# Kernel tuning notes

Measured on AMD Instinct MI355X. Metric: run time of the kernel, lower is better.

## Reference

```python
import jax, jax.numpy as jnp
import numpy as np

B, T, C = 4, 2048, 1024
NH = 16
HD = C // NH  # 64


def setup_inputs() -> dict:
    key = jax.random.key(0)
    k1, k2, k3, k4, k5 = jax.random.split(key, 5)
    s_in = 1.0 / np.sqrt(C)
    return {
        "x": jax.random.normal(k1, (B, T, C), dtype=jnp.float32),
        "attention_mask": jnp.ones((B, T), dtype=jnp.float32),
        "W_qkv": jax.random.normal(k2, (C, 3 * C), dtype=jnp.float32) * s_in,
        "b_qkv": jnp.zeros((3 * C,), dtype=jnp.float32),
        "W_out": jax.random.normal(k3, (C, C), dtype=jnp.float32) * s_in,
        "b_out": jnp.zeros((C,), dtype=jnp.float32),
    }


def reference(x, attention_mask, W_qkv, b_qkv, W_out, b_out):
    Bx, Tx, Cx = x.shape
    # QKV projection: (B,T,3C)
    qkv = x @ W_qkv + b_qkv
    Q, K, V = jnp.split(qkv, 3, axis=-1)
    # (B, NH, T, HD)
    Q = Q.reshape(Bx, Tx, NH, HD).transpose(0, 2, 1, 3)
    K = K.reshape(Bx, Tx, NH, HD).transpose(0, 2, 1, 3)
    V = V.reshape(Bx, Tx, NH, HD).transpose(0, 2, 1, 3)
    # scaled scores (B, NH, T, T)
    scores = jnp.einsum("bhqd,bhkd->bhqk", Q, K) * (1.0 / np.sqrt(HD))
    # causal mask: set strictly-upper triangle to -inf (mask-fill semantics)
    causal = jnp.tril(jnp.ones((Tx, Tx), dtype=bool))[None, None]
    scores = jnp.where(causal, scores, -jnp.inf)
    # additive padding mask
    pad = (1.0 - attention_mask)[:, None, None, :] * jnp.finfo(scores.dtype).min
    scores = scores + pad
    attn = jax.nn.softmax(scores, axis=-1)
    # weighted values -> (B, T, C)
    wv = jnp.einsum("bhqk,bhkd->bhqd", attn, V)
    wv = wv.transpose(0, 2, 1, 3).reshape(Bx, Tx, Cx)
    return wv @ W_out + b_out
```

## Files before the change

kernel.cpp:

```cpp
#include <hip/hip_runtime.h>
#include <math.h>

constexpr int BB = 4;
constexpr int TT = 2048;
constexpr int CC = 1024;
constexpr int NHH = 16;
constexpr int HDD = 64;
constexpr int C3 = 3 * CC;

typedef __bf16 bf16x8 __attribute__((ext_vector_type(8)));
typedef __bf16 bf16x4 __attribute__((ext_vector_type(4)));
typedef float  f32x4  __attribute__((ext_vector_type(4)));

__device__ __forceinline__ unsigned short f2bf(float x) {
    union { float f; unsigned u; } v; v.f = x;
    unsigned r = v.u + 0x7fffu + ((v.u >> 16) & 1u);
    return (unsigned short)(r >> 16);
}

#define AS1(p) ((const __attribute__((address_space(1))) void*)(p))
#define AS3(p) ((__attribute__((address_space(3))) void*)(p))

constexpr float SM2 = 17.312340490667561f;

constexpr int CAST_BLOCKS = (BB * TT * CC / 4) / 256;
constexpr int TQKV_BLOCKS = (C3 / 64) * (CC / 64);
constexpr int TOUT_BLOCKS = (CC / 64) * (CC / 64);
constexpr int KB_BLOCKS   = (BB * TT) / 256;

__global__ __launch_bounds__(256) void prep(
    const float* __restrict__ x,
    const float* __restrict__ Wqkv,
    const float* __restrict__ Wout,
    const float* __restrict__ amask,
    unsigned short* __restrict__ xb,
    unsigned short* __restrict__ Wqkvt,
    unsigned short* __restrict__ Woutt,
    float* __restrict__ kbias)
{
    __shared__ float tile[64][65];
    const int bid = blockIdx.x;
    const int t = threadIdx.x;

    if (bid < CAST_BLOCKS) {
        const int i = bid * 256 + t;
        float4 v = ((const float4*)x)[i];
        ushort4 o;
        o.x = f2bf(v.x); o.y = f2bf(v.y); o.z = f2bf(v.z); o.w = f2bf(v.w);
        ((ushort4*)xb)[i] = o;
        return;
    }
    if (bid >= CAST_BLOCKS + TQKV_BLOCKS + TOUT_BLOCKS) {
        const int i = (bid - CAST_BLOCKS - TQKV_BLOCKS - TOUT_BLOCKS) * 256 + t;
        kbias[i] = (amask[i] - 1.0f) * 1.0e38f - SM2;
        return;
    }

    const float* src; unsigned short* dst; int R, Cn, r0, c0;
    if (bid < CAST_BLOCKS + TQKV_BLOCKS) {
        const int tb = bid - CAST_BLOCKS;
        src = Wqkv; dst = Wqkvt; R = CC; Cn = C3;
        c0 = (tb % (C3 / 64)) * 64; r0 = (tb / (C3 / 64)) * 64;
    } else {
        const int tb = bid - CAST_BLOCKS - TQKV_BLOCKS;
        src = Wout; dst = Woutt; R = CC; Cn = CC;
        c0 = (tb % (CC / 64)) * 64; r0 = (tb / (CC / 64)) * 64;
    }

    const int lr = t >> 4, lc = (t & 15) * 4;
    #pragma unroll
    for (int s = 0; s < 4; ++s) {
        float4 v = *(const float4*)&src[(size_t)(r0 + lr + s * 16) * Cn + c0 + lc];
        tile[lr + s * 16][lc + 0] = v.x;
        tile[lr + s * 16][lc + 1] = v.y;
        tile[lr + s * 16][lc + 2] = v.z;
        tile[lr + s * 16][lc + 3] = v.w;
    }
    __syncthreads();
    const int oi = t >> 2, oc = (t & 3) * 16;
    unsigned short buf[16];
    #pragma unroll
    for (int u = 0; u < 16; ++u)
        buf[u] = f2bf(tile[oc + u][oi]);
    unsigned short* d = &dst[(size_t)(c0 + oi) * R + r0 + oc];
    *(uint4*)(d + 0) = *(uint4*)&buf[0];
    *(uint4*)(d + 8) = *(uint4*)&buf[8];
}

template<bool VSPLIT>
__global__ __launch_bounds__(256, 2) void gemm_bt_mfma(
    const unsigned short* __restrict__ A,
    const unsigned short* __restrict__ Bt,
    const float* __restrict__ bias,
    float* __restrict__ OutF,
    unsigned short* __restrict__ Qp,
    unsigned short* __restrict__ Kp,
    unsigned short* __restrict__ Vtp,
    int M, int N, int K, float qscale)
{
    __shared__ alignas(16) unsigned short As[2][128 * 64];
    __shared__ alignas(16) unsigned short Bs[2][128 * 64];

    const int tid  = threadIdx.x;
    const int w    = tid >> 6;
    const int lane = tid & 63;
    const int quad = lane >> 4;
    const int col  = lane & 15;

    const int nX  = gridDim.x;
    const int lin = blockIdx.y * nX + blockIdx.x;
    const int pos = lin >> 3;
    const int mt  = ((lin & 7) << 3) | (pos & 7);
    const int nt  = pos >> 3;
    const int m0 = mt * 128, n0 = nt * 128;
    const int wr = w >> 1, wc = w & 1;

    f32x4 acc[4][4];
    #pragma unroll
    for (int i = 0; i < 4; ++i)
        #pragma unroll
        for (int j = 0; j < 4; ++j)
            #pragma unroll
            for (int r = 0; r < 4; ++r)
                acc[i][j][r] = 0.0f;

    const int srow = tid >> 3;
    const int spos = tid & 7;
    char* AsB = (char*)&As[0][0];
    char* BsB = (char*)&Bs[0][0];

    const int nk = K >> 6;

    auto DMA = [&](int kt, int buf) {
        const int k0 = kt << 6;
        #pragma unroll
        for (int i = 0; i < 4; ++i) {
            const int row = srow + 32 * i;
            const int sch = spos ^ (row & 7);
            __builtin_amdgcn_global_load_lds(
                AS1(A + (size_t)(m0 + row) * K + k0 + sch * 8),
                AS3(AsB + buf * 16384 + i * 4096 + w * 1024), 16, 0, 0);
            __builtin_amdgcn_global_load_lds(
                AS1(Bt + (size_t)(n0 + row) * K + k0 + sch * 8),
                AS3(BsB + buf * 16384 + i * 4096 + w * 1024), 16, 0, 0);
        }
    };

    DMA(0, 0);
    DMA(1, 1);
    asm volatile("s_waitcnt vmcnt(8)" ::: "memory");
    __builtin_amdgcn_s_barrier();

    for (int kt = 0; kt < nk; ++kt) {
        const int cur = kt & 1;
        const unsigned short* as = &As[cur][0];
        const unsigned short* bs = &Bs[cur][0];

        #pragma unroll
        for (int ks = 0; ks < 2; ++ks) {
            bf16x8 af[4], bf[4];
            #pragma unroll
            for (int i = 0; i < 4; ++i) {
                const int ra = wr * 64 + i * 16 + col;
                const int pa = ((quad + ks * 4) ^ (ra & 7)) * 8;
                af[i] = *(const bf16x8*)&as[ra * 64 + pa];
                const int rb = wc * 64 + i * 16 + col;
                const int pb = ((quad + ks * 4) ^ (rb & 7)) * 8;
                bf[i] = *(const bf16x8*)&bs[rb * 64 + pb];
            }
            #pragma unroll
            for (int i = 0; i < 4; ++i)
                #pragma unroll
                for (int j = 0; j < 4; ++j)
                    acc[i][j] = __builtin_amdgcn_mfma_f32_16x16x32_bf16(af[i], bf[j], acc[i][j], 0, 0, 0);
        }

        __builtin_amdgcn_s_barrier();
        if (kt + 2 < nk) {
            DMA(kt + 2, cur);
            asm volatile("s_waitcnt vmcnt(8)" ::: "memory");
        } else {
            asm volatile("s_waitcnt vmcnt(0)" ::: "memory");
        }
        __builtin_amdgcn_s_barrier();
    }

    if (VSPLIT) {
        if (n0 < CC) {
            #pragma unroll
            for (int i = 0; i < 4; ++i)
                #pragma unroll
                for (int r = 0; r < 4; ++r) {
                    const int m = m0 + wr * 64 + i * 16 + quad * 4 + r;
                    #pragma unroll
                    for (int j = 0; j < 4; ++j) {
                        const int n = n0 + wc * 64 + j * 16 + col;
                        Qp[(size_t)m * CC + n] = f2bf((acc[i][j][r] + bias[n]) * qscale);
                    }
                }
        } else if (n0 < 2 * CC) {
            #pragma unroll
            for (int i = 0; i < 4; ++i) {
                const int mb   = m0 + wr * 64 + i * 16 + quad * 4;
                const int bidx = mb >> 11;
                const int tloc = mb & 2047;
                #pragma unroll
                for (int j = 0; j < 4; ++j) {
                    const int n  = n0 + wc * 64 + j * 16 + col;
                    const int hh = (n - CC) >> 6;
                    const int dd = (n - CC) & 63;
                    #pragma unroll
                    for (int r = 0; r < 4; ++r)
                        Kp[(((size_t)bidx * NHH + hh) * TT + tloc + r) * HDD + dd] =
                            f2bf(acc[i][j][r] + bias[n]);
                }
            }
        } else {
            #pragma unroll
            for (int i = 0; i < 4; ++i) {
                const int mb   = m0 + wr * 64 + i * 16 + quad * 4;
                const int bidx = mb >> 11;
                const int tloc = mb & 2047;
                const int ktile = tloc >> 6, tc = tloc & 63;
                #pragma unroll
                for (int j = 0; j < 4; ++j) {
                    const int n  = n0 + wc * 64 + j * 16 + col;
                    const int hh = (n - 2 * CC) >> 6;
                    const int dd = (n - 2 * CC) & 63;
                    unsigned short pk[4];
                    #pragma unroll
                    for (int r = 0; r < 4; ++r)
                        pk[r] = f2bf(acc[i][j][r] + bias[n]);
                    *(uint2*)&Vtp[((((size_t)bidx * NHH + hh) * 32 + ktile) * HDD + dd) * 64 + tc] =
                        *(const uint2*)pk;
                }
            }
        }
    } else {
        #pragma unroll
        for (int i = 0; i < 4; ++i)
            #pragma unroll
            for (int r = 0; r < 4; ++r) {
                const int m = m0 + wr * 64 + i * 16 + quad * 4 + r;
                #pragma unroll
                for (int j = 0; j < 4; ++j) {
                    const int n = n0 + wc * 64 + j * 16 + col;
                    OutF[(size_t)m * N + n] = acc[i][j][r] + bias[n];
                }
            }
    }
}

constexpr int PP = 72;

__global__ __launch_bounds__(256, 3) void attn_mfma(
    const unsigned short* __restrict__ Qp,
    const unsigned short* __restrict__ Kp,
    const unsigned short* __restrict__ Vtp,
    const float* __restrict__ kbias,
    unsigned short* __restrict__ WV)
{
    __shared__ alignas(16) unsigned short Ks [2][64 * 64];
    __shared__ alignas(16) unsigned short Vts[2][64 * 64];
    __shared__ alignas(16) __bf16        Ps[4][32 * PP];

    const int tid  = threadIdx.x;
    const int w    = tid >> 6;
    const int lane = tid & 63;
    const int quad = lane >> 4;
    const int col  = lane & 15;

    const int gi = blockIdx.x;
    const int j  = gi >> 3;
    const int bh = ((gi & 7) << 3) | (j & 7);
    const int qb = 15 - (j >> 3);
    const int b = bh >> 4, h = bh & 15;

    const unsigned short* Qg = Qp + (size_t)b * TT * CC + (size_t)h * HDD;
    const unsigned short* Kg = Kp + (size_t)bh * TT * HDD;
    const unsigned short* Vg = Vtp + (size_t)bh * 32 * HDD * 64;
    const float* kb_g = kbias + b * TT;

    const int srow = tid >> 3;
    const int sch  = (tid & 7) ^ (srow & 7);
    char* KsB  = (char*)&Ks[0][0];
    char* VtsB = (char*)&Vts[0][0];

    const int qw = qb * 128 + w * 32;
    const int ntiles = 2 * qb + 2;

    bf16x8 qfa0 = *(const bf16x8*)(Qg + (size_t)(qw + col) * CC + quad * 8);
    bf16x8 qfa1 = *(const bf16x8*)(Qg + (size_t)(qw + col) * CC + 32 + quad * 8);
    bf16x8 qfb0 = *(const bf16x8*)(Qg + (size_t)(qw + 16 + col) * CC + quad * 8);
    bf16x8 qfb1 = *(const bf16x8*)(Qg + (size_t)(qw + 16 + col) * CC + 32 + quad * 8);

    f32x4 o[2][4];
    float l[2] = {0.0f, 0.0f};
    #pragma unroll
    for (int hh = 0; hh < 2; ++hh)
        #pragma unroll
        for (int t = 0; t < 4; ++t)
            #pragma unroll
            for (int r = 0; r < 4; ++r) o[hh][t][r] = 0.0f;

    auto DMA = [&](int tile, int buf) {
        #pragma unroll
        for (int i = 0; i < 2; ++i) {
            __builtin_amdgcn_global_load_lds(
                AS1(Kg + (size_t)(tile * 64 + srow + 32 * i) * HDD + sch * 8),
                AS3(KsB + buf * 8192 + i * 4096 + w * 1024), 16, 0, 0);
            __builtin_amdgcn_global_load_lds(
                AS1(Vg + ((size_t)tile * 64 + srow + 32 * i) * 64 + sch * 8),
                AS3(VtsB + buf * 8192 + i * 4096 + w * 1024), 16, 0, 0);
        }
    };

    f32x4 kbc[4], kbn[4];
    DMA(0, 0);
    #pragma unroll
    for (int t = 0; t < 4; ++t)
        kbc[t] = *(const f32x4*)&kb_g[t * 16 + quad * 4];
    DMA(1, 1);
    #pragma unroll
    for (int t = 0; t < 4; ++t)
        kbn[t] = *(const f32x4*)&kb_g[64 + t * 16 + quad * 4];
    asm volatile("s_waitcnt vmcnt(8)" ::: "memory");
    __builtin_amdgcn_s_barrier();

    for (int it = 0; it < ntiles; ++it) {
        const int kt  = it << 6;
        const int cur = it & 1;

        if (kt <= qw + 31) {
            const unsigned short* ksb = &Ks[cur][0];
            const unsigned short* vsb = &Vts[cur][0];

            f32x4 s[2][4];
            #pragma unroll
            for (int t = 0; t < 4; ++t) {
                const int row = t * 16 + col;
                const int c0 = (quad ^ (row & 7)) * 8;
                const int c1 = ((quad + 4) ^ (row & 7)) * 8;
                bf16x8 k0 = *(const bf16x8*)&ksb[row * 64 + c0];
                bf16x8 k1 = *(const bf16x8*)&ksb[row * 64 + c1];
                f32x4 za = __builtin_amdgcn_mfma_f32_16x16x32_bf16(k0, qfa0, kbc[t], 0, 0, 0);
                za = __builtin_amdgcn_mfma_f32_16x16x32_bf16(k1, qfa1, za, 0, 0, 0);
                s[0][t] = za;
                f32x4 zb = __builtin_amdgcn_mfma_f32_16x16x32_bf16(k0, qfb0, kbc[t], 0, 0, 0);
                zb = __builtin_amdgcn_mfma_f32_16x16x32_bf16(k1, qfb1, zb, 0, 0, 0);
                s[1][t] = zb;
            }

            const bool needc = (kt + 64 > qw);
            #pragma unroll
            for (int hh = 0; hh < 2; ++hh) {
                const int q = qw + hh * 16 + col;
                #pragma unroll
                for (int t = 0; t < 4; ++t) {
                    float pv[4];
                    #pragma unroll
                    for (int r = 0; r < 4; ++r) {
                        const int key = kt + t * 16 + quad * 4 + r;
                        float p = __builtin_amdgcn_exp2f(s[hh][t][r]);
                        if (needc && key > q) p = 0.0f;
                        l[hh] += p;
                        pv[r] = p;
                    }
                    bf16x4 pk4 = { (__bf16)pv[0], (__bf16)pv[1],
                                   (__bf16)pv[2], (__bf16)pv[3] };
                    *(bf16x4*)&Ps[w][(hh * 16 + col) * PP + t * 16 + quad * 4] = pk4;
                }
            }

            bf16x8 pa0 = *(const bf16x8*)&Ps[w][col * PP + quad * 8];
            bf16x8 pa1 = *(const bf16x8*)&Ps[w][col * PP + 32 + quad * 8];
            bf16x8 pb0 = *(const bf16x8*)&Ps[w][(16 + col) * PP + quad * 8];
            bf16x8 pb1 = *(const bf16x8*)&Ps[w][(16 + col) * PP + 32 + quad * 8];
            #pragma unroll
            for (int t = 0; t < 4; ++t) {
                const int row = t * 16 + col;
                const int c0 = (quad ^ (row & 7)) * 8;
                const int c1 = ((quad + 4) ^ (row & 7)) * 8;
                bf16x8 v0 = *(const bf16x8*)&vsb[row * 64 + c0];
                bf16x8 v1 = *(const bf16x8*)&vsb[row * 64 + c1];
                o[0][t] = __builtin_amdgcn_mfma_f32_16x16x32_bf16(pa0, v0, o[0][t], 0, 0, 0);
                o[0][t] = __builtin_amdgcn_mfma_f32_16x16x32_bf16(pa1, v1, o[0][t], 0, 0, 0);
                o[1][t] = __builtin_amdgcn_mfma_f32_16x16x32_bf16(pb0, v0, o[1][t], 0, 0, 0);
                o[1][t] = __builtin_amdgcn_mfma_f32_16x16x32_bf16(pb1, v1, o[1][t], 0, 0, 0);
            }
        }

        __builtin_amdgcn_s_barrier();

        #pragma unroll
        for (int t = 0; t < 4; ++t) kbc[t] = kbn[t];

        if (it + 2 < ntiles) {
            DMA(it + 2, cur);
            #pragma unroll
            for (int t = 0; t < 4; ++t)
                kbn[t] = *(const f32x4*)&kb_g[(it + 2) * 64 + t * 16 + quad * 4];
            asm volatile("s_waitcnt vmcnt(8)" ::: "memory");
        } else {
            asm volatile("s_waitcnt vmcnt(0)" ::: "memory");
        }
        __builtin_amdgcn_s_barrier();
    }

    #pragma unroll
    for (int hh = 0; hh < 2; ++hh) {
        l[hh] += __shfl_xor(l[hh], 16);
        l[hh] += __shfl_xor(l[hh], 32);
    }
    #pragma unroll
    for (int hh = 0; hh < 2; ++hh) {
        #pragma unroll
        for (int r = 0; r < 4; ++r) {
            const float Lr = __shfl(l[hh], (lane & 48) | (quad * 4 + r));
            const float inv = 1.0f / Lr;
            const int q = qw + hh * 16 + quad * 4 + r;
            unsigned short* dst = WV + ((size_t)b * TT + q) * CC + (size_t)h * HDD;
            #pragma unroll
            for (int t = 0; t < 4; ++t)
                dst[t * 16 + col] = f2bf(o[hh][t][r] * inv);
        }
    }
}

extern "C" void kernel_launch(void* const* d_in, const int* in_sizes, int n_in,
                              void* d_out, int out_size, void* d_ws, size_t ws_size,
                              hipStream_t stream) {
    const float* x     = (const float*)d_in[0];
    const float* amask = (const float*)d_in[1];
    const float* Wqkv  = (const float*)d_in[2];
    const float* bqkv  = (const float*)d_in[3];
    const float* Wout  = (const float*)d_in[4];
    const float* bout  = (const float*)d_in[5];
    float* out = (float*)d_out;

    const int M = BB * TT;

    unsigned short* xb    = (unsigned short*)d_ws;
    unsigned short* Wqkvt = xb    + (size_t)M * CC;
    unsigned short* Woutt = Wqkvt + (size_t)C3 * CC;
    unsigned short* Qp    = Woutt + (size_t)CC * CC;
    unsigned short* Kp    = Qp    + (size_t)M * CC;
    unsigned short* Vtp   = Kp    + (size_t)M * CC;
    unsigned short* wvb   = Vtp   + (size_t)M * CC;
    float*          kbias = (float*)(wvb + (size_t)M * CC);

    dim3 blk(256);

    prep<<<dim3(CAST_BLOCKS + TQKV_BLOCKS + TOUT_BLOCKS + KB_BLOCKS), blk, 0, stream>>>(
        x, Wqkv, Wout, amask, xb, Wqkvt, Woutt, kbias);

    gemm_bt_mfma<true><<<dim3(C3 / 128, M / 128), blk, 0, stream>>>(
        xb, Wqkvt, bqkv, nullptr, Qp, Kp, Vtp, M, C3, CC, 0.18033688011112043f);
    attn_mfma<<<dim3(1024), dim3(256), 0, stream>>>(
        Qp, Kp, Vtp, kbias, wvb);
    gemm_bt_mfma<false><<<dim3(CC / 128, M / 128), blk, 0, stream>>>(
        wvb, Woutt, bout, out, nullptr, nullptr, nullptr, M, CC, CC, 1.0f);
}
```

Measured before the change: 234.7 us.

## Load GEMM B operand directly from global into registers, bypassing LDS

The GEMM kernel no longer stages the B tile through shared memory. Each wave loads its own 64-column slice of B straight into register fragments one k-tile ahead, using ping-pong register buffers and a loop unrolled by two. This halves LDS traffic and footprint, and the LDS reads of B go away. In exchange it costs more VGPRs and issues less coalesced global loads, since both waves in a row pair fetch their B slices separately. The vmcnt waits are also retuned, and their counting with the mixed load types is fragile.

```diff
diff --git a/kernel.cpp b/kernel.cpp
--- a/kernel.cpp
+++ b/kernel.cpp
@@ -99,7 +99,6 @@
     int M, int N, int K, float qscale)
 {
     __shared__ alignas(16) unsigned short As[2][128 * 64];
-    __shared__ alignas(16) unsigned short Bs[2][128 * 64];
 
     const int tid  = threadIdx.x;
     const int w    = tid >> 6;
@@ -127,63 +126,89 @@
     const int srow = tid >> 3;
     const int spos = tid & 7;
     char* AsB = (char*)&As[0][0];
-    char* BsB = (char*)&Bs[0][0];
 
     const int nk = K >> 6;
+
+    const unsigned short* Bw = Bt + (size_t)(n0 + wc * 64) * K;
 
     auto DMA = [&](int kt, int buf) {
         const int k0 = kt << 6;
         #pragma unroll
         for (int i = 0; i < 4; ++i) {
             const int row = srow + 32 * i;
-            const int sch = spos ^ (row & 7);
+            const int sc = spos ^ (row & 7);
             __builtin_amdgcn_global_load_lds(
-                AS1(A + (size_t)(m0 + row) * K + k0 + sch * 8),
+                AS1(A + (size_t)(m0 + row) * K + k0 + sc * 8),
                 AS3(AsB + buf * 16384 + i * 4096 + w * 1024), 16, 0, 0);
-            __builtin_amdgcn_global_load_lds(
-                AS1(Bt + (size_t)(n0 + row) * K + k0 + sch * 8),
-                AS3(BsB + buf * 16384 + i * 4096 + w * 1024), 16, 0, 0);
         }
     };
 
+    #define LOADB(dst, T) { \
+        const int kk0 = ((T) << 6); \
+        _Pragma("unroll") \
+        for (int j = 0; j < 4; ++j) { \
+            const unsigned short* bp = Bw + (size_t)(j * 16 + col) * K + kk0 + quad * 8; \
+            dst[j * 2 + 0] = *(const bf16x8*)(bp); \
+            dst[j * 2 + 1] = *(const bf16x8*)(bp + 32); \
+        } }
+
+    #define COMPUTE(buf, bfr) { \
+        const unsigned short* as = &As[buf][0]; \
+        _Pragma("unroll") \
+        for (int ks = 0; ks < 2; ++ks) { \
+            bf16x8 af[4]; \
+            _Pragma("unroll") \
+            for (int i = 0; i < 4; ++i) { \
+                const int ra = wr * 64 + i * 16 + col; \
+                const int pa = ((quad + ks * 4) ^ (ra & 7)) * 8; \
+                af[i] = *(const bf16x8*)&as[ra * 64 + pa]; \
+            } \
+            _Pragma("unroll") \
+            for (int i = 0; i < 4; ++i) \
+                _Pragma("unroll") \
+                for (int j = 0; j < 4; ++j) \
+                    acc[i][j] = __builtin_amdgcn_mfma_f32_16x16x32_bf16(af[i], bfr[j * 2 + ks], acc[i][j], 0, 0, 0); \
+        } }
+
+    bf16x8 bfA[8], bfB[8];
+
+    LOADB(bfA, 0);
     DMA(0, 0);
     DMA(1, 1);
-    asm volatile("s_waitcnt vmcnt(8)" ::: "memory");
+    asm volatile("s_waitcnt vmcnt(4)" ::: "memory");
     __builtin_amdgcn_s_barrier();
 
-    for (int kt = 0; kt < nk; ++kt) {
-        const int cur = kt & 1;
-        const unsigned short* as = &As[cur][0];
-        const unsigned short* bs = &Bs[cur][0];
-
-        #pragma unroll
-        for (int ks = 0; ks < 2; ++ks) {
-            bf16x8 af[4], bf[4];
-            #pragma unroll
-            for (int i = 0; i < 4; ++i) {
-                const int ra = wr * 64 + i * 16 + col;
-                const int pa = ((quad + ks * 4) ^ (ra & 7)) * 8;
-                af[i] = *(const bf16x8*)&as[ra * 64 + pa];
-                const int rb = wc * 64 + i * 16 + col;
-                const int pb = ((quad + ks * 4) ^ (rb & 7)) * 8;
-                bf[i] = *(const bf16x8*)&bs[rb * 64 + pb];
-            }
-            #pragma unroll
-            for (int i = 0; i < 4; ++i)
-                #pragma unroll
-                for (int j = 0; j < 4; ++j)
-                    acc[i][j] = __builtin_amdgcn_mfma_f32_16x16x32_bf16(af[i], bf[j], acc[i][j], 0, 0, 0);
-        }
-
+    for (int kt = 0; kt < nk; kt += 2) {
+        if (kt + 1 < nk) LOADB(bfB, kt + 1);
+        COMPUTE(0, bfA);
         __builtin_amdgcn_s_barrier();
         if (kt + 2 < nk) {
-            DMA(kt + 2, cur);
+            DMA(kt + 2, 0);
+            asm volatile("s_waitcnt vmcnt(12)" ::: "memory");
+        } else if (kt + 1 < nk) {
             asm volatile("s_waitcnt vmcnt(8)" ::: "memory");
         } else {
             asm volatile("s_waitcnt vmcnt(0)" ::: "memory");
         }
         __builtin_amdgcn_s_barrier();
-    }
+
+        if (kt + 1 < nk) {
+            if (kt + 2 < nk) LOADB(bfA, kt + 2);
+            COMPUTE(1, bfB);
+            __builtin_amdgcn_s_barrier();
+            if (kt + 3 < nk) {
+                DMA(kt + 3, 1);
+                asm volatile("s_waitcnt vmcnt(12)" ::: "memory");
+            } else if (kt + 2 < nk) {
+                asm volatile("s_waitcnt vmcnt(8)" ::: "memory");
+            } else {
+                asm volatile("s_waitcnt vmcnt(0)" ::: "memory");
+            }
+            __builtin_amdgcn_s_barrier();
+        }
+    }
+    #undef LOADB
+    #undef COMPUTE
 
     if (VSPLIT) {
         if (n0 < CC) {
```

Result: slower. 308.6 us (+31.5%).

## Use 128x256 tiles with per-wave full-M layout in QKV GEMM

Applied to the files above, without the earlier changes.

The QKV projection GEMM gets its own kernel with a 128x256 output tile, where each wave owns a 128x64 column strip (8x4 MFMA accumulators) instead of a 64x64 quadrant. The wider tile halves the block count to 768 and raises arithmetic intensity per LDS byte, and the block-to-tile mapping groups M tiles by XCD for L2 reuse. The cost is 48KB LDS per buffer pair, launch bounds of 1 block per CU, and roughly 128 accumulator registers per thread, which lowers occupancy and latency hiding. The output GEMM is split off as a separate non-templated kernel with unchanged behaviour.

```diff
diff --git a/kernel.cpp b/kernel.cpp
--- a/kernel.cpp
+++ b/kernel.cpp
@@ -22,6 +22,7 @@
 #define AS3(p) ((__attribute__((address_space(3))) void*)(p))
 
 constexpr float SM2 = 17.312340490667561f;
+constexpr float QSCALE = 0.18033688011112043f;
 
 constexpr int CAST_BLOCKS = (BB * TT * CC / 4) / 256;
 constexpr int TQKV_BLOCKS = (C3 / 64) * (CC / 64);
@@ -87,16 +88,164 @@
     *(uint4*)(d + 8) = *(uint4*)&buf[8];
 }
 
-template<bool VSPLIT>
-__global__ __launch_bounds__(256, 2) void gemm_bt_mfma(
+__global__ __launch_bounds__(256, 1) void gemm_qkv(
+    const unsigned short* __restrict__ A,
+    const unsigned short* __restrict__ Bt,
+    const float* __restrict__ bias,
+    unsigned short* __restrict__ Qp,
+    unsigned short* __restrict__ Kp,
+    unsigned short* __restrict__ Vtp)
+{
+    __shared__ alignas(16) unsigned short As[2][128 * 64];
+    __shared__ alignas(16) unsigned short Bs[2][256 * 64];
+
+    const int tid  = threadIdx.x;
+    const int w    = tid >> 6;
+    const int lane = tid & 63;
+    const int quad = lane >> 4;
+    const int col  = lane & 15;
+
+    const int lin = blockIdx.x;
+    const int xcd = lin & 7, idx = lin >> 3;
+    const int mt  = xcd * 8 + (idx & 7);
+    const int nt  = idx >> 3;
+    const int m0 = mt * 128, n0 = nt * 256;
+
+    f32x4 acc[8][4];
+    #pragma unroll
+    for (int i = 0; i < 8; ++i)
+        #pragma unroll
+        for (int j = 0; j < 4; ++j)
+            #pragma unroll
+            for (int r = 0; r < 4; ++r)
+                acc[i][j][r] = 0.0f;
+
+    const int srow8 = lane >> 3;
+    const int sch   = (lane & 7) ^ srow8;
+    char* AsB = (char*)&As[0][0];
+    char* BsB = (char*)&Bs[0][0];
+
+    constexpr int K  = CC;
+    constexpr int nk = K / 64;
+
+    auto STAGE = [&](int kt, int buf) {
+        const int k0 = kt << 6;
+        #pragma unroll
+        for (int i = 0; i < 4; ++i) {
+            const int row = w * 32 + i * 8 + srow8;
+            __builtin_amdgcn_global_load_lds(
+                AS1(A + (size_t)(m0 + row) * K + k0 + sch * 8),
+                AS3(AsB + buf * 16384 + w * 4096 + i * 1024), 16, 0, 0);
+        }
+        #pragma unroll
+        for (int i = 0; i < 8; ++i) {
+            const int row = w * 64 + i * 8 + srow8;
+            __builtin_amdgcn_global_load_lds(
+                AS1(Bt + (size_t)(n0 + row) * K + k0 + sch * 8),
+                AS3(BsB + buf * 32768 + w * 8192 + i * 1024), 16, 0, 0);
+        }
+    };
+
+    STAGE(0, 0);
+    STAGE(1, 1);
+    asm volatile("s_waitcnt vmcnt(12)" ::: "memory");
+    __builtin_amdgcn_s_barrier();
+
+    for (int kt = 0; kt < nk; ++kt) {
+        const int cur = kt & 1;
+        const unsigned short* as = &As[cur][0];
+        const unsigned short* bs = &Bs[cur][0];
+
+        #pragma unroll
+        for (int ks = 0; ks < 2; ++ks) {
+            bf16x8 af[8], bf[4];
+            #pragma unroll
+            for (int i = 0; i < 8; ++i) {
+                const int ra = i * 16 + col;
+                const int pa = ((quad + ks * 4) ^ (ra & 7)) * 8;
+                af[i] = *(const bf16x8*)&as[ra * 64 + pa];
+            }
+            #pragma unroll
+            for (int j = 0; j < 4; ++j) {
+                const int rb = w * 64 + j * 16 + col;
+                const int pb = ((quad + ks * 4) ^ (rb & 7)) * 8;
+                bf[j] = *(const bf16x8*)&bs[rb * 64 + pb];
+            }
+            #pragma unroll
+            for (int i = 0; i < 8; ++i)
+                #pragma unroll
+                for (int j = 0; j < 4; ++j)
+                    acc[i][j] = __builtin_amdgcn_mfma_f32_16x16x32_bf16(af[i], bf[j], acc[i][j], 0, 0, 0);
+        }
+
+        __builtin_amdgcn_s_barrier();
+        if (kt + 2 < nk) {
+            STAGE(kt + 2, cur);
+            asm volatile("s_waitcnt vmcnt(12)" ::: "memory");
+        } else {
+            asm volatile("s_waitcnt vmcnt(0)" ::: "memory");
+        }
+        __builtin_amdgcn_s_barrier();
+    }
+
+    if (n0 < CC) {
+        #pragma unroll
+        for (int i = 0; i < 8; ++i)
+            #pragma unroll
+            for (int r = 0; r < 4; ++r) {
+                const int m = m0 + i * 16 + quad * 4 + r;
+                #pragma unroll
+                for (int j = 0; j < 4; ++j) {
+                    const int n = n0 + w * 64 + j * 16 + col;
+                    Qp[(size_t)m * CC + n] = f2bf((acc[i][j][r] + bias[n]) * QSCALE);
+                }
+            }
+    } else if (n0 < 2 * CC) {
+        #pragma unroll
+        for (int i = 0; i < 8; ++i) {
+            const int mb   = m0 + i * 16 + quad * 4;
+            const int bidx = mb >> 11;
+            const int tloc = mb & 2047;
+            #pragma unroll
+            for (int j = 0; j < 4; ++j) {
+                const int n  = n0 + w * 64 + j * 16 + col;
+                const int hh = (n - CC) >> 6;
+                const int dd = (n - CC) & 63;
+                #pragma unroll
+                for (int r = 0; r < 4; ++r)
+                    Kp[(((size_t)bidx * NHH + hh) * TT + tloc + r) * HDD + dd] =
+                        f2bf(acc[i][j][r] + bias[n]);
+            }
+        }
+    } else {
+        #pragma unroll
+        for (int i = 0; i < 8; ++i) {
+            const int mb   = m0 + i * 16 + quad * 4;
+            const int bidx = mb >> 11;
+            const int tloc = mb & 2047;
+            const int ktile = tloc >> 6, tc = tloc & 63;
+            #pragma unroll
+            for (int j = 0; j < 4; ++j) {
+                const int n  = n0 + w * 64 + j * 16 + col;
+                const int hh = (n - 2 * CC) >> 6;
+                const int dd = (n - 2 * CC) & 63;
+                unsigned short pk[4];
+                #pragma unroll
+                for (int r = 0; r < 4; ++r)
+                    pk[r] = f2bf(acc[i][j][r] + bias[n]);
+                *(uint2*)&Vtp[((((size_t)bidx * NHH + hh) * 32 + ktile) * HDD + dd) * 64 + tc] =
+                    *(const uint2*)pk;
+            }
+        }
+    }
+}
+
+__global__ __launch_bounds__(256, 2) void gemm_out(
     const unsigned short* __restrict__ A,
     const unsigned short* __restrict__ Bt,
     const float* __restrict__ bias,
     float* __restrict__ OutF,
-    unsigned short* __restrict__ Qp,
-    unsigned short* __restrict__ Kp,
-    unsigned short* __restrict__ Vtp,
-    int M, int N, int K, float qscale)
+    int M, int N, int K)
 {
     __shared__ alignas(16) unsigned short As[2][128 * 64];
     __shared__ alignas(16) unsigned short Bs[2][128 * 64];
@@ -136,12 +285,12 @@
         #pragma unroll
         for (int i = 0; i < 4; ++i) {
             const int row = srow + 32 * i;
-            const int sch = spos ^ (row & 7);
+            const int sc = spos ^ (row & 7);
             __builtin_amdgcn_global_load_lds(
-                AS1(A + (size_t)(m0 + row) * K + k0 + sch * 8),
+                AS1(A + (size_t)(m0 + row) * K + k0 + sc * 8),
                 AS3(AsB + buf * 16384 + i * 4096 + w * 1024), 16, 0, 0);
             __builtin_amdgcn_global_load_lds(
-                AS1(Bt + (size_t)(n0 + row) * K + k0 + sch * 8),
+                AS1(Bt + (size_t)(n0 + row) * K + k0 + sc * 8),
                 AS3(BsB + buf * 16384 + i * 4096 + w * 1024), 16, 0, 0);
         }
     };
@@ -185,70 +334,17 @@
         __builtin_amdgcn_s_barrier();
     }
 
-    if (VSPLIT) {
-        if (n0 < CC) {
-            #pragma unroll
-            for (int i = 0; i < 4; ++i)
-                #pragma unroll
-                for (int r = 0; r < 4; ++r) {
-                    const int m = m0 + wr * 64 + i * 16 + quad * 4 + r;
-                    #pragma unroll
-                    for (int j = 0; j < 4; ++j) {
-                        const int n = n0 + wc * 64 + j * 16 + col;
-                        Qp[(size_t)m * CC + n] = f2bf((acc[i][j][r] + bias[n]) * qscale);
-                    }
-                }
-        } else if (n0 < 2 * CC) {
-            #pragma unroll
-            for (int i = 0; i < 4; ++i) {
-                const int mb   = m0 + wr * 64 + i * 16 + quad * 4;
-                const int bidx = mb >> 11;
-                const int tloc = mb & 2047;
-                #pragma unroll
-                for (int j = 0; j < 4; ++j) {
-                    const int n  = n0 + wc * 64 + j * 16 + col;
-                    const int hh = (n - CC) >> 6;
-                    const int dd = (n - CC) & 63;
-                    #pragma unroll
-                    for (int r = 0; r < 4; ++r)
-                        Kp[(((size_t)bidx * NHH + hh) * TT + tloc + r) * HDD + dd] =
-                            f2bf(acc[i][j][r] + bias[n]);
-                }
-            }
-        } else {
-            #pragma unroll
-            for (int i = 0; i < 4; ++i) {
-                const int mb   = m0 + wr * 64 + i * 16 + quad * 4;
-                const int bidx = mb >> 11;
-                const int tloc = mb & 2047;
-                const int ktile = tloc >> 6, tc = tloc & 63;
-                #pragma unroll
-                for (int j = 0; j < 4; ++j) {
-                    const int n  = n0 + wc * 64 + j * 16 + col;
-                    const int hh = (n - 2 * CC) >> 6;
-                    const int dd = (n - 2 * CC) & 63;
-                    unsigned short pk[4];
-                    #pragma unroll
-                    for (int r = 0; r < 4; ++r)
-                        pk[r] = f2bf(acc[i][j][r] + bias[n]);
-                    *(uint2*)&Vtp[((((size_t)bidx * NHH + hh) * 32 + ktile) * HDD + dd) * 64 + tc] =
-                        *(const uint2*)pk;
-                }
-            }
-        }
-    } else {
-        #pragma unroll
-        for (int i = 0; i < 4; ++i)
-            #pragma unroll
-            for (int r = 0; r < 4; ++r) {
-                const int m = m0 + wr * 64 + i * 16 + quad * 4 + r;
-                #pragma unroll
-                for (int j = 0; j < 4; ++j) {
-                    const int n = n0 + wc * 64 + j * 16 + col;
-                    OutF[(size_t)m * N + n] = acc[i][j][r] + bias[n];
-                }
-            }
-    }
+    #pragma unroll
+    for (int i = 0; i < 4; ++i)
+        #pragma unroll
+        for (int r = 0; r < 4; ++r) {
+            const int m = m0 + wr * 64 + i * 16 + quad * 4 + r;
+            #pragma unroll
+            for (int j = 0; j < 4; ++j) {
+                const int n = n0 + wc * 64 + j * 16 + col;
+                OutF[(size_t)m * N + n] = acc[i][j][r] + bias[n];
+            }
+        }
 }
 
 constexpr int PP = 72;
@@ -454,10 +550,10 @@
     prep<<<dim3(CAST_BLOCKS + TQKV_BLOCKS + TOUT_BLOCKS + KB_BLOCKS), blk, 0, stream>>>(
         x, Wqkv, Wout, amask, xb, Wqkvt, Woutt, kbias);
 
-    gemm_bt_mfma<true><<<dim3(C3 / 128, M / 128), blk, 0, stream>>>(
-        xb, Wqkvt, bqkv, nullptr, Qp, Kp, Vtp, M, C3, CC, 0.18033688011112043f);
+    gemm_qkv<<<dim3(768), blk, 0, stream>>>(
+        xb, Wqkvt, bqkv, Qp, Kp, Vtp);
     attn_mfma<<<dim3(1024), dim3(256), 0, stream>>>(
         Qp, Kp, Vtp, kbias, wvb);
-    gemm_bt_mfma<false><<<dim3(CC / 128, M / 128), blk, 0, stream>>>(
-        wvb, Woutt, bout, out, nullptr, nullptr, nullptr, M, CC, CC, 1.0f);
+    gemm_out<<<dim3(CC / 128, M / 128), blk, 0, stream>>>(
+        wvb, Woutt, bout, out, M, CC, CC);
 }
```

Measured after the change: 270.4 us. 1.15x slower.

## Double attention block to 8 waves over 256 queries sharing K/V tiles

Applied to the files above, without the earlier changes.

The attention kernel now runs 512-thread blocks covering 256 query rows, so each K/V tile staged in LDS is reused by eight waves instead of four, and the grid shrinks to 512 blocks. Each thread now issues one DMA per K and V tile, and the wait counts are adjusted to match. The softmax loop is also split into a masked diagonal path and an unmasked path, which removes the per-element causal check on full tiles. In exchange, blocks are larger and there are fewer of them, causal load imbalance across blocks grows, and waves whose queries sit past a tile still wait at the barriers.

```diff
diff --git a/kernel.cpp b/kernel.cpp
--- a/kernel.cpp
+++ b/kernel.cpp
@@ -136,12 +136,12 @@
         #pragma unroll
         for (int i = 0; i < 4; ++i) {
             const int row = srow + 32 * i;
-            const int sch = spos ^ (row & 7);
+            const int sc = spos ^ (row & 7);
             __builtin_amdgcn_global_load_lds(
-                AS1(A + (size_t)(m0 + row) * K + k0 + sch * 8),
+                AS1(A + (size_t)(m0 + row) * K + k0 + sc * 8),
                 AS3(AsB + buf * 16384 + i * 4096 + w * 1024), 16, 0, 0);
             __builtin_amdgcn_global_load_lds(
-                AS1(Bt + (size_t)(n0 + row) * K + k0 + sch * 8),
+                AS1(Bt + (size_t)(n0 + row) * K + k0 + sc * 8),
                 AS3(BsB + buf * 16384 + i * 4096 + w * 1024), 16, 0, 0);
         }
     };
@@ -253,7 +253,7 @@
 
 constexpr int PP = 72;
 
-__global__ __launch_bounds__(256, 3) void attn_mfma(
+__global__ __launch_bounds__(512, 4) void attn_mfma(
     const unsigned short* __restrict__ Qp,
     const unsigned short* __restrict__ Kp,
     const unsigned short* __restrict__ Vtp,
@@ -262,7 +262,7 @@
 {
     __shared__ alignas(16) unsigned short Ks [2][64 * 64];
     __shared__ alignas(16) unsigned short Vts[2][64 * 64];
-    __shared__ alignas(16) __bf16        Ps[4][32 * PP];
+    __shared__ alignas(16) __bf16        Ps[8][32 * PP];
 
     const int tid  = threadIdx.x;
     const int w    = tid >> 6;
@@ -273,7 +273,7 @@
     const int gi = blockIdx.x;
     const int j  = gi >> 3;
     const int bh = ((gi & 7) << 3) | (j & 7);
-    const int qb = 15 - (j >> 3);
+    const int qb = 7 - (j >> 3);
     const int b = bh >> 4, h = bh & 15;
 
     const unsigned short* Qg = Qp + (size_t)b * TT * CC + (size_t)h * HDD;
@@ -286,8 +286,8 @@
     char* KsB  = (char*)&Ks[0][0];
     char* VtsB = (char*)&Vts[0][0];
 
-    const int qw = qb * 128 + w * 32;
-    const int ntiles = 2 * qb + 2;
+    const int qw = qb * 256 + w * 32;
+    const int ntiles = 4 * qb + 4;
 
     bf16x8 qfa0 = *(const bf16x8*)(Qg + (size_t)(qw + col) * CC + quad * 8);
     bf16x8 qfa1 = *(const bf16x8*)(Qg + (size_t)(qw + col) * CC + 32 + quad * 8);
@@ -304,15 +304,12 @@
             for (int r = 0; r < 4; ++r) o[hh][t][r] = 0.0f;
 
     auto DMA = [&](int tile, int buf) {
-        #pragma unroll
-        for (int i = 0; i < 2; ++i) {
-            __builtin_amdgcn_global_load_lds(
-                AS1(Kg + (size_t)(tile * 64 + srow + 32 * i) * HDD + sch * 8),
-                AS3(KsB + buf * 8192 + i * 4096 + w * 1024), 16, 0, 0);
-            __builtin_amdgcn_global_load_lds(
-                AS1(Vg + ((size_t)tile * 64 + srow + 32 * i) * 64 + sch * 8),
-                AS3(VtsB + buf * 8192 + i * 4096 + w * 1024), 16, 0, 0);
-        }
+        __builtin_amdgcn_global_load_lds(
+            AS1(Kg + (size_t)(tile * 64 + srow) * HDD + sch * 8),
+            AS3(KsB + buf * 8192 + w * 1024), 16, 0, 0);
+        __builtin_amdgcn_global_load_lds(
+            AS1(Vg + ((size_t)tile * 64 + srow) * 64 + sch * 8),
+            AS3(VtsB + buf * 8192 + w * 1024), 16, 0, 0);
     };
 
     f32x4 kbc[4], kbn[4];
@@ -324,7 +321,7 @@
     #pragma unroll
     for (int t = 0; t < 4; ++t)
         kbn[t] = *(const f32x4*)&kb_g[64 + t * 16 + quad * 4];
-    asm volatile("s_waitcnt vmcnt(8)" ::: "memory");
+    asm volatile("s_waitcnt vmcnt(6)" ::: "memory");
     __builtin_amdgcn_s_barrier();
 
     for (int it = 0; it < ntiles; ++it) {
@@ -351,24 +348,42 @@
                 s[1][t] = zb;
             }
 
-            const bool needc = (kt + 64 > qw);
-            #pragma unroll
-            for (int hh = 0; hh < 2; ++hh) {
-                const int q = qw + hh * 16 + col;
-                #pragma unroll
-                for (int t = 0; t < 4; ++t) {
-                    float pv[4];
+            if (kt + 64 > qw) {
+                #pragma unroll
+                for (int hh = 0; hh < 2; ++hh) {
+                    const int q = qw + hh * 16 + col;
                     #pragma unroll
-                    for (int r = 0; r < 4; ++r) {
-                        const int key = kt + t * 16 + quad * 4 + r;
-                        float p = __builtin_amdgcn_exp2f(s[hh][t][r]);
-                        if (needc && key > q) p = 0.0f;
-                        l[hh] += p;
-                        pv[r] = p;
+                    for (int t = 0; t < 4; ++t) {
+                        float pv[4];
+                        #pragma unroll
+                        for (int r = 0; r < 4; ++r) {
+                            const int key = kt + t * 16 + quad * 4 + r;
+                            float p = __builtin_amdgcn_exp2f(s[hh][t][r]);
+                            if (key > q) p = 0.0f;
+                            l[hh] += p;
+                            pv[r] = p;
+                        }
+                        bf16x4 pk4 = { (__bf16)pv[0], (__bf16)pv[1],
+                                       (__bf16)pv[2], (__bf16)pv[3] };
+                        *(bf16x4*)&Ps[w][(hh * 16 + col) * PP + t * 16 + quad * 4] = pk4;
                     }
-                    bf16x4 pk4 = { (__bf16)pv[0], (__bf16)pv[1],
-                                   (__bf16)pv[2], (__bf16)pv[3] };
-                    *(bf16x4*)&Ps[w][(hh * 16 + col) * PP + t * 16 + quad * 4] = pk4;
+                }
+            } else {
+                #pragma unroll
+                for (int hh = 0; hh < 2; ++hh) {
+                    #pragma unroll
+                    for (int t = 0; t < 4; ++t) {
+                        float pv[4];
+                        #pragma unroll
+                        for (int r = 0; r < 4; ++r) {
+                            float p = __builtin_amdgcn_exp2f(s[hh][t][r]);
+                            l[hh] += p;
+                            pv[r] = p;
+                        }
+                        bf16x4 pk4 = { (__bf16)pv[0], (__bf16)pv[1],
+                                       (__bf16)pv[2], (__bf16)pv[3] };
+                        *(bf16x4*)&Ps[w][(hh * 16 + col) * PP + t * 16 + quad * 4] = pk4;
+                    }
                 }
             }
 
@@ -400,7 +415,7 @@
             #pragma unroll
             for (int t = 0; t < 4; ++t)
                 kbn[t] = *(const f32x4*)&kb_g[(it + 2) * 64 + t * 16 + quad * 4];
-            asm volatile("s_waitcnt vmcnt(8)" ::: "memory");
+            asm volatile("s_waitcnt vmcnt(6)" ::: "memory");
         } else {
             asm volatile("s_waitcnt vmcnt(0)" ::: "memory");
         }
@@ -456,7 +471,7 @@
 
     gemm_bt_mfma<true><<<dim3(C3 / 128, M / 128), blk, 0, stream>>>(
         xb, Wqkvt, bqkv, nullptr, Qp, Kp, Vtp, M, C3, CC, 0.18033688011112043f);
-    attn_mfma<<<dim3(1024), dim3(256), 0, stream>>>(
+    attn_mfma<<<dim3(512), dim3(512), 0, stream>>>(
         Qp, Kp, Vtp, kbias, wvb);
     gemm_bt_mfma<false><<<dim3(CC / 128, M / 128), blk, 0, stream>>>(
         wvb, Woutt, bout, out, nullptr, nullptr, nullptr, M, CC, CC, 1.0f);
```

Result: slower. 288.4 us (+22.9%).
